# Optimization experiments

Measured on AMD Instinct MI355X. Metric: run time of the kernel, lower is better.

The kernel has to match this reference:

```python
import jax, jax.numpy as jnp
import numpy as np

D_MODEL = 2048
NUM_HEADS = 16
MAX_SEQ_LEN = 2048
ROPE_BASE = 10000.0


def _rope(x, start_pos):
    # x: [B, S, D]; rotates interleaved pairs then concatenates halves,
    # exactly matching the torch module (NOT the usual interleaved output).
    B, S, D = x.shape
    theta = 1.0 / (ROPE_BASE ** (jnp.arange(0, D, 2, dtype=jnp.float32) / D))  # [D/2]
    pos = jnp.arange(start_pos, start_pos + S, dtype=jnp.float32)[:, None]      # [S,1]
    ang = pos * theta[None, :]                                                  # [S, D/2]
    cos, sin = jnp.cos(ang), jnp.sin(ang)
    x1 = x[..., 0::2]
    x2 = x[..., 1::2]
    return jnp.concatenate([x1 * cos - x2 * sin, x1 * sin + x2 * cos], axis=-1)


def setup_inputs() -> dict:
    key = jax.random.key(0)
    kx, kq, kk, kv, ko = jax.random.split(key, 5)
    B, S, D = 4, 2048, D_MODEL
    scale = 1.0 / np.sqrt(D)
    return {
        "x": jax.random.normal(kx, (B, S, D), dtype=jnp.float32),
        "w_q": jax.random.normal(kq, (D, D), dtype=jnp.float32) * scale,
        "w_k": jax.random.normal(kk, (D, D), dtype=jnp.float32) * scale,
        "w_v": jax.random.normal(kv, (D, D), dtype=jnp.float32) * scale,
        "w_o": jax.random.normal(ko, (D, D), dtype=jnp.float32) * scale,
        "start_pos": 0,
    }


def reference(x, w_q, w_k, w_v, w_o, start_pos):
    B, S, D = x.shape
    H = NUM_HEADS
    hd = D // H
    # Linear(d, d, bias=False): y = x @ W^T
    Q = _rope(x @ w_q.T, start_pos)
    K = _rope(x @ w_k.T, start_pos)
    V = x @ w_v.T
    q = Q.reshape(B, S, H, hd).transpose(0, 2, 1, 3)  # [B,H,S,hd]
    k = K.reshape(B, S, H, hd).transpose(0, 2, 1, 3)
    v = V.reshape(B, S, H, hd).transpose(0, 2, 1, 3)
    # cache=None path: kv_len == S
    attn = jnp.einsum("bhqd,bhkd->bhqk", q, k) / jnp.sqrt(jnp.float32(hd))
    # causal mask: key j attends only if j <= i + (kv_len - seq_len); here offset=0
    kv_len = k.shape[2]
    offset = kv_len - S
    i = jnp.arange(S)[:, None]
    j = jnp.arange(kv_len)[None, :]
    attn = jnp.where(j > i + offset, jnp.float32(-jnp.inf), attn)
    attn = jax.nn.softmax(attn, axis=-1)
    # dropout: inference mode (identity)
    out = jnp.einsum("bhqk,bhkd->bhqd", attn, v)
    out = out.transpose(0, 2, 1, 3).reshape(B, S, D)
    output = out @ w_o.T
    return (output, k, v)
```

## Files before the change

kernel.cpp:

```cpp
#include <hip/hip_runtime.h>
#include <hip/hip_bf16.h>

typedef __attribute__((ext_vector_type(4))) float f32x4;
typedef __attribute__((ext_vector_type(8))) short s16x8;

#define SEQ 2048
#define DM  2048
#define NH  16
#define HD  128

__device__ __forceinline__ unsigned short f2b(float f){
  unsigned int u = __builtin_bit_cast(unsigned int, f);
  u += 0x7fffu + ((u >> 16) & 1u);
  return (unsigned short)(u >> 16);
}
__device__ __forceinline__ float b2f(unsigned short h){
  unsigned int u = ((unsigned int)h) << 16;
  return __builtin_bit_cast(float, u);
}
__device__ __forceinline__ f32x4 mfma16(s16x8 a, s16x8 b, f32x4 c){
  return __builtin_amdgcn_mfma_f32_16x16x32_bf16(a, b, c, 0, 0, 0);
}

__global__ __launch_bounds__(256)
void convert_kernel(const float* __restrict__ x,  const float* __restrict__ wq,
                    const float* __restrict__ wk, const float* __restrict__ wv,
                    const float* __restrict__ wo,
                    unsigned short* __restrict__ xb,
                    unsigned short* __restrict__ wfused,
                    unsigned short* __restrict__ wob)
{
  size_t e = ((size_t)blockIdx.x * 256 + threadIdx.x) * 8;
  const float* src; unsigned short* dst;
  if (e < 16777216){ src = x + e; dst = xb + e; }
  else if (e < 29360128){
    size_t o = e - 16777216;
    int sel = (int)(o >> 22);
    const float* w = sel == 0 ? wq : (sel == 1 ? wk : wv);
    src = w + (o & 4194303); dst = wfused + o;
  } else {
    size_t o = e - 29360128;
    src = wo + o; dst = wob + o;
  }
  float4 a = ((const float4*)src)[0];
  float4 b = ((const float4*)src)[1];
  s16x8 v;
  v[0]=(short)f2b(a.x); v[1]=(short)f2b(a.y); v[2]=(short)f2b(a.z); v[3]=(short)f2b(a.w);
  v[4]=(short)f2b(b.x); v[5]=(short)f2b(b.y); v[6]=(short)f2b(b.z); v[7]=(short)f2b(b.w);
  *(s16x8*)dst = v;
}

__global__ __launch_bounds__(256)
void upconv_kernel(const unsigned short* __restrict__ src, float* __restrict__ dst)
{
  size_t e = ((size_t)blockIdx.x * 256 + threadIdx.x) * 8;
  s16x8 v = *(const s16x8*)(src + e);
  f32x4 a, b;
  #pragma unroll
  for (int i = 0; i < 4; i++){
    a[i] = b2f((unsigned short)v[i]);
    b[i] = b2f((unsigned short)v[i+4]);
  }
  *(f32x4*)(dst + e)     = a;
  *(f32x4*)(dst + e + 4) = b;
}

template<int MODE>
__global__ __launch_bounds__(512, 1)
void gemm8(const unsigned short* __restrict__ A,
           const unsigned short* __restrict__ B,
           unsigned short* __restrict__ qr, unsigned short* __restrict__ kr,
           float* __restrict__ voutf, unsigned short* __restrict__ vt,
           float* __restrict__ outf, const int* __restrict__ sp)
{
  extern __shared__ char lds[];
  const int tid  = threadIdx.x;
  const int lane = tid & 63;
  const int w    = tid >> 6;
  const int wr   = w >> 2;
  const int wc   = w & 3;
  const int l15  = lane & 15;
  const int lhi  = lane >> 4;
  const int rq   = lhi << 2;

  int bid = blockIdx.x;
  int x8 = bid & 7, jb = bid >> 3;
  int mb, nb;
  if (MODE == 0){ nb = 3*x8 + (jb % 3); mb = jb / 3; }
  else          { nb = x8;              mb = jb; }
  const int m0 = mb * 256, n0 = nb * 256;

  const int sp0 = (MODE == 0) ? sp[0] : 0;

  const unsigned short* Abase = A + (size_t)m0 * 2048;
  const unsigned short* Bbase = B + (size_t)n0 * 2048;

  f32x4 accL[4][4] = {};
  f32x4 accH[4][4] = {};

  auto STAGE = [&](const unsigned short* gbase, int slotoff, int t){
    #pragma unroll
    for (int r2 = 0; r2 < 2; r2++){
      int p  = r2*8192 + w*1024 + (lane << 4);
      int lo = p ^ (((p >> 7) & 3) << 4);
      int row = lo >> 6, colB = lo & 63;
      __builtin_amdgcn_global_load_lds(
        (const __attribute__((address_space(1))) void*)
          (gbase + (size_t)row*2048 + t*32 + (colB >> 1)),
        (__attribute__((address_space(3))) void*)(lds + slotoff + r2*8192 + w*1024),
        16, 0, 0);
    }
  };
  auto LDA = [&](const char* base, int i0, s16x8* dst){
    #pragma unroll
    for (int i = 0; i < 4; i++){
      int row = wr*128 + (i0 + i)*16 + l15;
      int off = row*64 + lhi*16;
      dst[i] = *(const s16x8*)(base + (off ^ (((row >> 1) & 3) << 4)));
    }
  };
  auto LDB = [&](const char* base, s16x8* dst){
    #pragma unroll
    for (int j2 = 0; j2 < 4; j2++){
      int row = wc*64 + j2*16 + l15;
      int off = row*64 + lhi*16;
      dst[j2] = *(const s16x8*)(base + (off ^ (((row >> 1) & 3) << 4)));
    }
  };
  auto MM = [&](s16x8* a, s16x8* b, f32x4 (&ac)[4][4]){
    __builtin_amdgcn_s_setprio(1);
    #pragma unroll
    for (int i = 0; i < 4; i++)
      #pragma unroll
      for (int j2 = 0; j2 < 4; j2++)
        ac[i][j2] = mfma16(a[i], b[j2], ac[i][j2]);
    __builtin_amdgcn_s_setprio(0);
  };

#define TILE(T, ISSUE, VMW) { \
    const int s_ = (T) & 3; \
    const char* base_ = lds + s_*32768; \
    if (ISSUE){ \
      int so_ = (((T)+3) & 3)*32768; \
      STAGE(Abase, so_, (T)+3); \
      STAGE(Bbase, so_+16384, (T)+3); \
    } \
    s16x8 bfr[4], afL[4], afH[4]; \
    LDB(base_+16384, bfr); LDA(base_, 0, afL); LDA(base_, 4, afH); \
    MM(afL, bfr, accL); MM(afH, bfr, accH); \
    asm volatile("s_waitcnt vmcnt(" #VMW ")" ::: "memory"); \
    __builtin_amdgcn_s_barrier(); }

  STAGE(Abase, 0, 0);      STAGE(Bbase, 16384, 0);
  STAGE(Abase, 32768, 1);  STAGE(Bbase, 49152, 1);
  STAGE(Abase, 65536, 2);  STAGE(Bbase, 81920, 2);
  asm volatile("s_waitcnt vmcnt(8)" ::: "memory");
  __builtin_amdgcn_s_barrier();

  for (int t = 0; t < 61; t++) TILE(t, 1, 8);
  TILE(61, 0, 4);
  TILE(62, 0, 0);
  {
    const char* base_ = lds + 3*32768;
    s16x8 bfr[4], afL[4], afH[4];
    LDB(base_+16384, bfr); LDA(base_, 0, afL); LDA(base_, 4, afH);
    MM(afL, bfr, accL); MM(afH, bfr, accH);
  }
#undef TILE

  if (MODE == 1){
    #pragma unroll
    for (int h2 = 0; h2 < 2; h2++){
      f32x4 (&ac)[4][4] = h2 ? accH : accL;
      int ibase = h2 * 4;
      #pragma unroll
      for (int i = 0; i < 4; i++)
        #pragma unroll
        for (int r = 0; r < 4; r++){
          int m = m0 + wr*128 + (ibase+i)*16 + rq + r;
          #pragma unroll
          for (int j2 = 0; j2 < 4; j2++)
            outf[(size_t)m*DM + n0 + wc*64 + j2*16 + l15] = ac[i][j2][r];
        }
    }
    return;
  }

  const int b  = m0 >> 11;
  const int s0 = m0 & 2047;

  if (nb < 16){
    const bool isK = (nb >= 8);
    unsigned short* dqk = isK ? kr : qr;
    const int fbase = (nb & 7) * 128;
    const int odd = lane & 1;

    __syncthreads();
    float2* T2 = (float2*)lds;
    float2* T1 = (float2*)(lds + 32768);
    for (int idx = tid; idx < 5120; idx += 512){
      int fl = idx & 127;
      float th = exp2f(-(float)(fbase + fl) * (13.287712379549449f / 1024.0f));
      float sn, cn;
      if (idx < 4096){
        __sincosf((float)(idx >> 7) * th, &sn, &cn);
        T2[idx] = make_float2(cn, sn);
      } else {
        int sh = (idx - 4096) >> 7;
        __sincosf((float)(sp0 + s0 + sh*32) * th, &sn, &cn);
        T1[idx - 4096] = make_float2(cn, sn);
      }
    }
    __syncthreads();

    #pragma unroll
    for (int h2 = 0; h2 < 2; h2++){
      f32x4 (&ac)[4][4] = h2 ? accH : accL;
      int ibase = h2 * 4;
      #pragma unroll
      for (int i = 0; i < 4; i++){
        #pragma unroll
        for (int r = 0; r < 4; r++){
          int srow = wr*128 + (ibase+i)*16 + rq + r;
          int s  = s0 + srow;
          int sh = srow >> 5, sl = srow & 31;
          #pragma unroll
          for (int j2 = 0; j2 < 4; j2++){
            float v  = ac[i][j2][r];
            float vx = __shfl_xor(v, 1);
            int nn_loc = wc*64 + j2*16 + l15;
            int fl = nn_loc >> 1;
            float2 a1 = T1[sh*128 + fl];
            float2 a2 = T2[sl*128 + fl];
            float cn = a1.x*a2.x - a1.y*a2.y;
            float sn = a1.y*a2.x + a1.x*a2.y;
            float x1 = odd ? vx : v;
            float x2 = odd ? v  : vx;
            float ov = odd ? (x1*sn + x2*cn) : (x1*cn - x2*sn);
            int c = fbase + fl + (odd ? 1024 : 0);
            size_t adr = ((size_t)(b*NH + (c >> 7))*SEQ + s)*HD + (c & 127);
            dqk[adr] = f2b(ov);
          }
        }
      }
    }
  } else {
    #pragma unroll
    for (int h2 = 0; h2 < 2; h2++){
      f32x4 (&ac)[4][4] = h2 ? accH : accL;
      int ibase = h2 * 4;
      #pragma unroll
      for (int i = 0; i < 4; i++){
        int sb = s0 + wr*128 + (ibase+i)*16 + rq;
        #pragma unroll
        for (int j2 = 0; j2 < 4; j2++){
          int d = (nb - 16)*256 + wc*64 + j2*16 + l15;
          int h = d >> 7, dd = d & 127;
          size_t vb = ((size_t)(b*NH + h)*SEQ + sb)*HD + dd;
          #pragma unroll
          for (int r = 0; r < 4; r++)
            voutf[vb + (size_t)r*HD] = ac[i][j2][r];
          ushort4 pk;
          pk.x = f2b(ac[i][j2][0]); pk.y = f2b(ac[i][j2][1]);
          pk.z = f2b(ac[i][j2][2]); pk.w = f2b(ac[i][j2][3]);
          *(ushort4*)(vt + ((size_t)(b*NH + h)*HD + dd)*SEQ + sb) = pk;
        }
      }
    }
  }
}

__global__ __launch_bounds__(256)
void attn_kernel(const unsigned short* __restrict__ qr,
                 const unsigned short* __restrict__ kr,
                 const unsigned short* __restrict__ vt,
                 unsigned short* __restrict__ attnout)
{
  const int pair = blockIdx.x;
  const int bh   = blockIdx.y;
  const int tid  = threadIdx.x;
  const int lane = tid & 63;
  const int w    = tid >> 6;

  __shared__ __align__(16) char Klds[64 * 256];
  __shared__ __align__(16) char Vlds[128 * 144];
  __shared__ __align__(16) char Plds[4][16 * 144];

  const int l15 = lane & 15;
  const int lhi = lane >> 4;
  const int rq  = lhi << 2;
  char* pw = &Plds[w][0];

  s16x8 ones;
  #pragma unroll
  for (int i = 0; i < 8; i++) ones[i] = (short)0x3F80;

  const int b = bh >> 4, h = bh & 15;

  for (int ph = 0; ph < 2; ph++){
    const int qtile = ph ? (31 - pair) : pair;
    const int q0w = qtile*64 + w*16;

    s16x8 qf[4];
    const unsigned short* qbase = qr + ((size_t)bh*SEQ + q0w + l15) * HD + lhi*8;
    #pragma unroll
    for (int c = 0; c < 4; c++) qf[c] = *(const s16x8*)(qbase + c*32);

    f32x4 o[8] = {};
    f32x4 osum = {};
    float mrow[4] = {-1e30f,-1e30f,-1e30f,-1e30f};

    const int ntiles = qtile + 1;
    for (int t = 0; t < ntiles; t++){
      const int kv0 = t * 64;
      __syncthreads();
      {
        int r = tid >> 2, q4 = tid & 3;
        const unsigned short* src = kr + ((size_t)bh*SEQ + kv0 + r) * HD + q4*32;
        int sw = (r & 15) << 4;
        char* drow = Klds + r*256;
        #pragma unroll
        for (int k = 0; k < 4; k++)
          *(s16x8*)(drow + ((q4*64 + k*16) ^ sw)) = *(const s16x8*)(src + k*8);
      }
      {
        int r = tid >> 1, h2 = tid & 1;
        const unsigned short* src = vt + ((size_t)bh*HD + r) * SEQ + kv0 + h2*32;
        char* drow = Vlds + r*144 + h2*64;
        #pragma unroll
        for (int k = 0; k < 4; k++)
          *(s16x8*)(drow + k*16) = *(const s16x8*)(src + k*8);
      }
      __syncthreads();

      f32x4 st[4];
      #pragma unroll
      for (int j = 0; j < 4; j++) st[j] = (f32x4){0.f,0.f,0.f,0.f};
      #pragma unroll
      for (int j = 0; j < 4; j++){
        int krw = j*16 + l15;
        int sw  = (krw & 15) << 4;
        #pragma unroll
        for (int c = 0; c < 4; c++){
          s16x8 kf = *(const s16x8*)(Klds + krw*256 + ((c*64 + lhi*16) ^ sw));
          st[j] = mfma16(qf[c], kf, st[j]);
        }
      }

      const float sc = 0.08838834764831845f;
      #pragma unroll
      for (int j = 0; j < 4; j++)
        #pragma unroll
        for (int r = 0; r < 4; r++){
          int qrow = q0w + rq + r;
          int kvc  = kv0 + j*16 + l15;
          st[j][r] = (kvc > qrow) ? -1e30f : st[j][r] * sc;
        }

      float mt[4];
      #pragma unroll
      for (int r = 0; r < 4; r++)
        mt[r] = fmaxf(fmaxf(st[0][r], st[1][r]), fmaxf(st[2][r], st[3][r]));
      #pragma unroll
      for (int mk = 1; mk < 16; mk <<= 1)
        #pragma unroll
        for (int r = 0; r < 4; r++) mt[r] = fmaxf(mt[r], __shfl_xor(mt[r], mk));

      int ok = 1;
      #pragma unroll
      for (int r = 0; r < 4; r++) ok &= (mt[r] <= mrow[r] + 8.0f) ? 1 : 0;
      if (!__all(ok)){
        float al[4];
        #pragma unroll
        for (int r = 0; r < 4; r++){
          float mn = fmaxf(mrow[r], mt[r]);
          al[r] = __expf(mrow[r] - mn);
          mrow[r] = mn;
        }
        #pragma unroll
        for (int c = 0; c < 8; c++)
          #pragma unroll
          for (int r = 0; r < 4; r++) o[c][r] *= al[r];
        #pragma unroll
        for (int r = 0; r < 4; r++) osum[r] *= al[r];
      }

      #pragma unroll
      for (int r = 0; r < 4; r++){
        char* prb = pw + (rq + r)*144;
        #pragma unroll
        for (int j = 0; j < 4; j++){
          float p = __expf(st[j][r] - mrow[r]);
          *(unsigned short*)(prb + (j*16 + l15)*2) = f2b(p);
        }
      }

      asm volatile("s_waitcnt lgkmcnt(0)" ::: "memory");

      #pragma unroll
      for (int ks = 0; ks < 2; ks++){
        s16x8 pa = *(const s16x8*)(pw + l15*144 + ks*64 + lhi*16);
        #pragma unroll
        for (int c = 0; c < 8; c++){
          int d = c*16 + l15;
          s16x8 vf = *(const s16x8*)(Vlds + d*144 + ks*64 + lhi*16);
          o[c] = mfma16(pa, vf, o[c]);
        }
        osum = mfma16(pa, ones, osum);
      }
    }

    #pragma unroll
    for (int r = 0; r < 4; r++){
      float inv = 1.0f / osum[r];
      int s2 = q0w + rq + r;
      size_t base = ((size_t)(b*SEQ + s2)) * DM + h*HD;
      #pragma unroll
      for (int c = 0; c < 8; c++)
        attnout[base + c*16 + l15] = f2b(o[c][r] * inv);
    }
  }
}

extern "C" void kernel_launch(void* const* d_in, const int* in_sizes, int n_in,
                              void* d_out, int out_size, void* d_ws, size_t ws_size,
                              hipStream_t stream)
{
  const float* x  = (const float*)d_in[0];
  const float* wq = (const float*)d_in[1];
  const float* wk = (const float*)d_in[2];
  const float* wv = (const float*)d_in[3];
  const float* wo = (const float*)d_in[4];
  const int*   sp = (const int*)d_in[5];

  float* out  = (float*)d_out;
  float* kout = out + 16777216;
  float* vout = out + 33554432;

  char* ws = (char*)d_ws;
  unsigned short* xb      = (unsigned short*)ws;
  unsigned short* wfused  = (unsigned short*)(ws + 33554432);
  unsigned short* wob     = (unsigned short*)(ws + 58720256);
  unsigned short* qr      = (unsigned short*)(ws + 67108864);
  unsigned short* kr      = (unsigned short*)(ws + 100663296);
  unsigned short* vt      = (unsigned short*)(ws + 134217728);
  unsigned short* attnout = (unsigned short*)ws;

  hipFuncSetAttribute((const void*)gemm8<0>,
                      hipFuncAttributeMaxDynamicSharedMemorySize, 131072);
  hipFuncSetAttribute((const void*)gemm8<1>,
                      hipFuncAttributeMaxDynamicSharedMemorySize, 131072);

  convert_kernel<<<16384, 256, 0, stream>>>(x, wq, wk, wv, wo, xb, wfused, wob);
  gemm8<0><<<768, 512, 131072, stream>>>(xb, wfused, qr, kr,
                                         vout, vt, nullptr, sp);
  upconv_kernel<<<8192, 256, 0, stream>>>(kr, kout);
  attn_kernel<<<dim3(16, 64), 256, 0, stream>>>(qr, kr, vt, attnout);
  gemm8<1><<<256, 512, 131072, stream>>>(attnout, wob, nullptr, nullptr,
                                         nullptr, nullptr, out, nullptr);
}
```

Before: 524.4 us.

## Enlarge attention q-tile to 128 rows, fuse K upconversion, add MFMA priority

The attention kernel now processes 128 query rows per block, with each wave handling two 16-row subtiles. Each K/V tile loaded into LDS is therefore reused across twice as many queries, and the grid is halved. The separate bf16-to-fp32 K output upconversion kernel is removed and its work folded into the attention kernel's epilogue, saving a launch and one pass over K. s_setprio hints are added around the MFMA loops. The costs are higher register pressure, fewer blocks to balance the causal work, and diagonal tiles that now do more masked work.

```diff
diff --git a/kernel.cpp b/kernel.cpp
--- a/kernel.cpp
+++ b/kernel.cpp
@@ -50,21 +50,6 @@
   *(s16x8*)dst = v;
 }
 
-__global__ __launch_bounds__(256)
-void upconv_kernel(const unsigned short* __restrict__ src, float* __restrict__ dst)
-{
-  size_t e = ((size_t)blockIdx.x * 256 + threadIdx.x) * 8;
-  s16x8 v = *(const s16x8*)(src + e);
-  f32x4 a, b;
-  #pragma unroll
-  for (int i = 0; i < 4; i++){
-    a[i] = b2f((unsigned short)v[i]);
-    b[i] = b2f((unsigned short)v[i+4]);
-  }
-  *(f32x4*)(dst + e)     = a;
-  *(f32x4*)(dst + e + 4) = b;
-}
-
 template<int MODE>
 __global__ __launch_bounds__(512, 1)
 void gemm8(const unsigned short* __restrict__ A,
@@ -274,7 +259,8 @@
 void attn_kernel(const unsigned short* __restrict__ qr,
                  const unsigned short* __restrict__ kr,
                  const unsigned short* __restrict__ vt,
-                 unsigned short* __restrict__ attnout)
+                 unsigned short* __restrict__ attnout,
+                 float* __restrict__ koutf)
 {
   const int pair = blockIdx.x;
   const int bh   = blockIdx.y;
@@ -284,7 +270,7 @@
 
   __shared__ __align__(16) char Klds[64 * 256];
   __shared__ __align__(16) char Vlds[128 * 144];
-  __shared__ __align__(16) char Plds[4][16 * 144];
+  __shared__ __align__(16) char Plds[4][32 * 144];
 
   const int l15 = lane & 15;
   const int lhi = lane >> 4;
@@ -298,19 +284,27 @@
   const int b = bh >> 4, h = bh & 15;
 
   for (int ph = 0; ph < 2; ph++){
-    const int qtile = ph ? (31 - pair) : pair;
-    const int q0w = qtile*64 + w*16;
-
-    s16x8 qf[4];
-    const unsigned short* qbase = qr + ((size_t)bh*SEQ + q0w + l15) * HD + lhi*8;
-    #pragma unroll
-    for (int c = 0; c < 4; c++) qf[c] = *(const s16x8*)(qbase + c*32);
-
-    f32x4 o[8] = {};
-    f32x4 osum = {};
-    float mrow[4] = {-1e30f,-1e30f,-1e30f,-1e30f};
-
-    const int ntiles = qtile + 1;
+    const int qtile = ph ? (15 - pair) : pair;
+    const int q0w = qtile*128 + w*32;
+
+    s16x8 qf[2][4];
+    #pragma unroll
+    for (int qt = 0; qt < 2; qt++){
+      const unsigned short* qbase =
+        qr + ((size_t)bh*SEQ + q0w + qt*16 + l15) * HD + lhi*8;
+      #pragma unroll
+      for (int c = 0; c < 4; c++) qf[qt][c] = *(const s16x8*)(qbase + c*32);
+    }
+
+    f32x4 o[2][8] = {};
+    f32x4 osum[2] = {};
+    float mrow[2][4];
+    #pragma unroll
+    for (int qt = 0; qt < 2; qt++)
+      #pragma unroll
+      for (int r = 0; r < 4; r++) mrow[qt][r] = -1e30f;
+
+    const int ntiles = 2*qtile + 2;
     for (int t = 0; t < ntiles; t++){
       const int kv0 = t * 64;
       __syncthreads();
@@ -333,9 +327,12 @@
       }
       __syncthreads();
 
-      f32x4 st[4];
-      #pragma unroll
-      for (int j = 0; j < 4; j++) st[j] = (f32x4){0.f,0.f,0.f,0.f};
+      f32x4 st[2][4];
+      #pragma unroll
+      for (int qt = 0; qt < 2; qt++)
+        #pragma unroll
+        for (int j = 0; j < 4; j++) st[qt][j] = (f32x4){0.f,0.f,0.f,0.f};
+      __builtin_amdgcn_s_setprio(1);
       #pragma unroll
       for (int j = 0; j < 4; j++){
         int krw = j*16 + l15;
@@ -343,81 +340,126 @@
         #pragma unroll
         for (int c = 0; c < 4; c++){
           s16x8 kf = *(const s16x8*)(Klds + krw*256 + ((c*64 + lhi*16) ^ sw));
-          st[j] = mfma16(qf[c], kf, st[j]);
-        }
-      }
+          st[0][j] = mfma16(qf[0][c], kf, st[0][j]);
+          st[1][j] = mfma16(qf[1][c], kf, st[1][j]);
+        }
+      }
+      __builtin_amdgcn_s_setprio(0);
 
       const float sc = 0.08838834764831845f;
       #pragma unroll
-      for (int j = 0; j < 4; j++)
+      for (int qt = 0; qt < 2; qt++)
+        #pragma unroll
+        for (int j = 0; j < 4; j++)
+          #pragma unroll
+          for (int r = 0; r < 4; r++){
+            int qrow = q0w + qt*16 + rq + r;
+            int kvc  = kv0 + j*16 + l15;
+            st[qt][j][r] = (kvc > qrow) ? -1e30f : st[qt][j][r] * sc;
+          }
+
+      float mt[2][4];
+      #pragma unroll
+      for (int qt = 0; qt < 2; qt++)
+        #pragma unroll
+        for (int r = 0; r < 4; r++)
+          mt[qt][r] = fmaxf(fmaxf(st[qt][0][r], st[qt][1][r]),
+                            fmaxf(st[qt][2][r], st[qt][3][r]));
+      #pragma unroll
+      for (int mk = 1; mk < 16; mk <<= 1)
+        #pragma unroll
+        for (int qt = 0; qt < 2; qt++)
+          #pragma unroll
+          for (int r = 0; r < 4; r++)
+            mt[qt][r] = fmaxf(mt[qt][r], __shfl_xor(mt[qt][r], mk));
+
+      int ok = 1;
+      #pragma unroll
+      for (int qt = 0; qt < 2; qt++)
+        #pragma unroll
+        for (int r = 0; r < 4; r++)
+          ok &= (mt[qt][r] <= mrow[qt][r] + 8.0f) ? 1 : 0;
+      if (!__all(ok)){
+        #pragma unroll
+        for (int qt = 0; qt < 2; qt++){
+          float al[4];
+          #pragma unroll
+          for (int r = 0; r < 4; r++){
+            float mn = fmaxf(mrow[qt][r], mt[qt][r]);
+            al[r] = __expf(mrow[qt][r] - mn);
+            mrow[qt][r] = mn;
+          }
+          #pragma unroll
+          for (int c = 0; c < 8; c++)
+            #pragma unroll
+            for (int r = 0; r < 4; r++) o[qt][c][r] *= al[r];
+          #pragma unroll
+          for (int r = 0; r < 4; r++) osum[qt][r] *= al[r];
+        }
+      }
+
+      #pragma unroll
+      for (int qt = 0; qt < 2; qt++)
         #pragma unroll
         for (int r = 0; r < 4; r++){
-          int qrow = q0w + rq + r;
-          int kvc  = kv0 + j*16 + l15;
-          st[j][r] = (kvc > qrow) ? -1e30f : st[j][r] * sc;
-        }
-
-      float mt[4];
-      #pragma unroll
-      for (int r = 0; r < 4; r++)
-        mt[r] = fmaxf(fmaxf(st[0][r], st[1][r]), fmaxf(st[2][r], st[3][r]));
-      #pragma unroll
-      for (int mk = 1; mk < 16; mk <<= 1)
-        #pragma unroll
-        for (int r = 0; r < 4; r++) mt[r] = fmaxf(mt[r], __shfl_xor(mt[r], mk));
-
-      int ok = 1;
-      #pragma unroll
-      for (int r = 0; r < 4; r++) ok &= (mt[r] <= mrow[r] + 8.0f) ? 1 : 0;
-      if (!__all(ok)){
-        float al[4];
-        #pragma unroll
-        for (int r = 0; r < 4; r++){
-          float mn = fmaxf(mrow[r], mt[r]);
-          al[r] = __expf(mrow[r] - mn);
-          mrow[r] = mn;
-        }
-        #pragma unroll
-        for (int c = 0; c < 8; c++)
-          #pragma unroll
-          for (int r = 0; r < 4; r++) o[c][r] *= al[r];
-        #pragma unroll
-        for (int r = 0; r < 4; r++) osum[r] *= al[r];
-      }
-
-      #pragma unroll
-      for (int r = 0; r < 4; r++){
-        char* prb = pw + (rq + r)*144;
-        #pragma unroll
-        for (int j = 0; j < 4; j++){
-          float p = __expf(st[j][r] - mrow[r]);
-          *(unsigned short*)(prb + (j*16 + l15)*2) = f2b(p);
-        }
-      }
+          char* prb = pw + (qt*16 + rq + r)*144;
+          #pragma unroll
+          for (int j = 0; j < 4; j++){
+            float p = __expf(st[qt][j][r] - mrow[qt][r]);
+            *(unsigned short*)(prb + (j*16 + l15)*2) = f2b(p);
+          }
+        }
 
       asm volatile("s_waitcnt lgkmcnt(0)" ::: "memory");
 
       #pragma unroll
       for (int ks = 0; ks < 2; ks++){
-        s16x8 pa = *(const s16x8*)(pw + l15*144 + ks*64 + lhi*16);
+        s16x8 pa[2];
+        #pragma unroll
+        for (int qt = 0; qt < 2; qt++)
+          pa[qt] = *(const s16x8*)(pw + (qt*16 + l15)*144 + ks*64 + lhi*16);
+        __builtin_amdgcn_s_setprio(1);
         #pragma unroll
         for (int c = 0; c < 8; c++){
           int d = c*16 + l15;
           s16x8 vf = *(const s16x8*)(Vlds + d*144 + ks*64 + lhi*16);
-          o[c] = mfma16(pa, vf, o[c]);
-        }
-        osum = mfma16(pa, ones, osum);
-      }
-    }
-
-    #pragma unroll
-    for (int r = 0; r < 4; r++){
-      float inv = 1.0f / osum[r];
-      int s2 = q0w + rq + r;
-      size_t base = ((size_t)(b*SEQ + s2)) * DM + h*HD;
-      #pragma unroll
-      for (int c = 0; c < 8; c++)
-        attnout[base + c*16 + l15] = f2b(o[c][r] * inv);
+          o[0][c] = mfma16(pa[0], vf, o[0][c]);
+          o[1][c] = mfma16(pa[1], vf, o[1][c]);
+        }
+        osum[0] = mfma16(pa[0], ones, osum[0]);
+        osum[1] = mfma16(pa[1], ones, osum[1]);
+        __builtin_amdgcn_s_setprio(0);
+      }
+    }
+
+    #pragma unroll
+    for (int qt = 0; qt < 2; qt++)
+      #pragma unroll
+      for (int r = 0; r < 4; r++){
+        float inv = 1.0f / osum[qt][r];
+        int s2 = q0w + qt*16 + rq + r;
+        size_t base = ((size_t)(b*SEQ + s2)) * DM + h*HD;
+        #pragma unroll
+        for (int c = 0; c < 8; c++)
+          attnout[base + c*16 + l15] = f2b(o[qt][c][r] * inv);
+      }
+
+    {
+      const unsigned short* ksrc = kr + ((size_t)bh*SEQ + qtile*128)*HD;
+      float* kdst = koutf + ((size_t)bh*SEQ + qtile*128)*HD;
+      #pragma unroll
+      for (int ch = 0; ch < 8; ch++){
+        size_t e = (size_t)ch*2048 + tid*8;
+        s16x8 v = *(const s16x8*)(ksrc + e);
+        f32x4 a2, b2;
+        #pragma unroll
+        for (int i = 0; i < 4; i++){
+          a2[i] = b2f((unsigned short)v[i]);
+          b2[i] = b2f((unsigned short)v[i+4]);
+        }
+        *(f32x4*)(kdst + e)     = a2;
+        *(f32x4*)(kdst + e + 4) = b2;
+      }
     }
   }
 }
@@ -454,8 +496,7 @@
   convert_kernel<<<16384, 256, 0, stream>>>(x, wq, wk, wv, wo, xb, wfused, wob);
   gemm8<0><<<768, 512, 131072, stream>>>(xb, wfused, qr, kr,
                                          vout, vt, nullptr, sp);
-  upconv_kernel<<<8192, 256, 0, stream>>>(kr, kout);
-  attn_kernel<<<dim3(16, 64), 256, 0, stream>>>(qr, kr, vt, attnout);
+  attn_kernel<<<dim3(8, 64), 256, 0, stream>>>(qr, kr, vt, attnout, kout);
   gemm8<1><<<256, 512, 131072, stream>>>(attnout, wob, nullptr, nullptr,
                                          nullptr, nullptr, out, nullptr);
 }
```

New measurement: 551.5 us. 5.2% more time.

## Fuse K fp32 upconversion into attention kernel and remap blocks per XCD

Applied to the files above, without the earlier changes.

Removes the separate upconv kernel that expanded bf16 K to fp32 output. Each attention block now also converts its 64-row K tile for the current qtile to fp32 after finishing its output. The block index is also remapped so that all blocks of a given batch-head land on the same XCD, which is meant to improve L2 reuse of K and V. Together these drop a kernel launch and a pass over K, at the cost of extra tail work inside the attention blocks.

```diff
diff --git a/kernel.cpp b/kernel.cpp
--- a/kernel.cpp
+++ b/kernel.cpp
@@ -50,21 +50,6 @@
   *(s16x8*)dst = v;
 }
 
-__global__ __launch_bounds__(256)
-void upconv_kernel(const unsigned short* __restrict__ src, float* __restrict__ dst)
-{
-  size_t e = ((size_t)blockIdx.x * 256 + threadIdx.x) * 8;
-  s16x8 v = *(const s16x8*)(src + e);
-  f32x4 a, b;
-  #pragma unroll
-  for (int i = 0; i < 4; i++){
-    a[i] = b2f((unsigned short)v[i]);
-    b[i] = b2f((unsigned short)v[i+4]);
-  }
-  *(f32x4*)(dst + e)     = a;
-  *(f32x4*)(dst + e + 4) = b;
-}
-
 template<int MODE>
 __global__ __launch_bounds__(512, 1)
 void gemm8(const unsigned short* __restrict__ A,
@@ -274,10 +259,14 @@
 void attn_kernel(const unsigned short* __restrict__ qr,
                  const unsigned short* __restrict__ kr,
                  const unsigned short* __restrict__ vt,
-                 unsigned short* __restrict__ attnout)
+                 unsigned short* __restrict__ attnout,
+                 float* __restrict__ koutf)
 {
-  const int pair = blockIdx.x;
-  const int bh   = blockIdx.y;
+  const int L    = (int)blockIdx.x + 16 * (int)blockIdx.y;
+  const int xcd  = L & 7;
+  const int idx  = L >> 3;
+  const int bh   = (xcd << 3) | (idx & 7);
+  const int pair = idx >> 3;
   const int tid  = threadIdx.x;
   const int lane = tid & 63;
   const int w    = tid >> 6;
@@ -418,6 +407,24 @@
       #pragma unroll
       for (int c = 0; c < 8; c++)
         attnout[base + c*16 + l15] = f2b(o[c][r] * inv);
+    }
+
+    {
+      const unsigned short* ksrc = kr + ((size_t)bh*SEQ + qtile*64)*HD;
+      float* kdst = koutf + ((size_t)bh*SEQ + qtile*64)*HD;
+      #pragma unroll
+      for (int ch = 0; ch < 4; ch++){
+        size_t e = (size_t)ch*2048 + tid*8;
+        s16x8 v = *(const s16x8*)(ksrc + e);
+        f32x4 a2, b2;
+        #pragma unroll
+        for (int i = 0; i < 4; i++){
+          a2[i] = b2f((unsigned short)v[i]);
+          b2[i] = b2f((unsigned short)v[i+4]);
+        }
+        *(f32x4*)(kdst + e)     = a2;
+        *(f32x4*)(kdst + e + 4) = b2;
+      }
     }
   }
 }
@@ -454,8 +461,7 @@
   convert_kernel<<<16384, 256, 0, stream>>>(x, wq, wk, wv, wo, xb, wfused, wob);
   gemm8<0><<<768, 512, 131072, stream>>>(xb, wfused, qr, kr,
                                          vout, vt, nullptr, sp);
-  upconv_kernel<<<8192, 256, 0, stream>>>(kr, kout);
-  attn_kernel<<<dim3(16, 64), 256, 0, stream>>>(qr, kr, vt, attnout);
+  attn_kernel<<<dim3(16, 64), 256, 0, stream>>>(qr, kr, vt, attnout, kout);
   gemm8<1><<<256, 512, 131072, stream>>>(attnout, wob, nullptr, nullptr,
                                          nullptr, nullptr, out, nullptr);
 }
```

Result: faster. 503.7 us, median of 2 (-4.0%).
